# Kernel tuning notes

Hardware: AMD Instinct MI355X
Metric: run time of the kernel (lower is better)

## Reference

```python
import jax, jax.numpy as jnp
import numpy as np

EMBED_DIM = 1024
NUM_HEADS = 16
HEAD_DIM = EMBED_DIM // NUM_HEADS
STD = 0.02


def setup_inputs() -> dict:
    key = jax.random.key(0)
    k1, k2, k3 = jax.random.split(key, 3)
    B, S = 2, 2048
    inputs = jax.random.normal(k1, (B, S, EMBED_DIM), dtype=jnp.float32)
    # qkv projection: Linear(E, 3E); torch Linear weight is [out, in]
    w_qkv = jax.random.normal(k2, (3 * EMBED_DIM, EMBED_DIM), dtype=jnp.float32) * STD
    b_qkv = jnp.zeros((3 * EMBED_DIM,), dtype=jnp.float32)
    w_out = jax.random.normal(k3, (EMBED_DIM, EMBED_DIM), dtype=jnp.float32) * STD
    b_out = jnp.zeros((EMBED_DIM,), dtype=jnp.float32)
    return {"inputs": inputs, "w_qkv": w_qkv, "b_qkv": b_qkv, "w_out": w_out, "b_out": b_out}


def reference(inputs, w_qkv, b_qkv, w_out, b_out):
    B, S, E = inputs.shape
    qkv = inputs @ w_qkv.T + b_qkv                      # [B,S,3E]
    q, k, v = jnp.split(qkv, 3, axis=2)                 # each [B,S,E]

    def split_heads(t):
        return t.reshape(B, S, NUM_HEADS, HEAD_DIM).transpose(0, 2, 1, 3)  # [B,H,S,D]

    q, k, v = split_heads(q), split_heads(k), split_heads(v)
    scores = jnp.einsum('bhqd,bhkd->bhqk', q, k) * (1.0 / np.sqrt(HEAD_DIM))
    causal = jnp.tril(jnp.ones((S, S), dtype=bool))     # [S,S]
    scores = jnp.where(causal[None, None, :, :], scores, -jnp.inf)
    probs = jax.nn.softmax(scores, axis=-1)             # dropout is identity in eval mode
    ctx = jnp.einsum('bhqk,bhkd->bhqd', probs, v)       # [B,H,S,D]
    ctx = ctx.transpose(0, 2, 1, 3).reshape(B, S, E)
    return ctx @ w_out.T + b_out
```

## Files before the change

kernel.cpp:

```cpp
#include <hip/hip_runtime.h>
#include <hip/hip_bf16.h>

#define BATCH 2
#define SEQ   2048
#define EMB   1024
#define NHEAD 16
#define HDIM  64
#define MTOT  (BATCH*SEQ)
#define KTOT  EMB

#define NX  (MTOT*EMB)
#define NW1 (3*EMB*EMB)
#define NW2 (EMB*EMB)
#define NCVT (NX+NW1+NW2)

typedef short bf8 __attribute__((ext_vector_type(8)));
typedef short s4v __attribute__((ext_vector_type(4)));
typedef float f4  __attribute__((ext_vector_type(4)));
typedef unsigned int uint;

__device__ __forceinline__ short f2b(float f) {
    __hip_bfloat16 h = __float2bfloat16(f);
    return __builtin_bit_cast(short, h);
}
__device__ __forceinline__ void gl_lds16(const short* g, short* l) {
    __builtin_amdgcn_global_load_lds(
        (const __attribute__((address_space(1))) uint*)g,
        (__attribute__((address_space(3))) uint*)l, 16, 0, 0);
}
#define SWZ_SRC(lane)      ((((lane) ^ ((lane)>>2) ^ ((lane)>>4)) & 3) * 8)
#define SWZ_RD(quad, l16)  ((((quad) ^ (l16) ^ ((l16)>>2)) & 3) * 8)

__global__ __launch_bounds__(256) void cvt_all(
    const float* __restrict__ X, const float* __restrict__ W1,
    const float* __restrict__ W2,
    short* __restrict__ xb, short* __restrict__ w1b, short* __restrict__ w2b)
{
    int i4 = (blockIdx.x * 256 + threadIdx.x) * 4;
    const float* src; short* dst; int off;
    if (i4 < NX)            { src = X;  dst = xb;  off = i4; }
    else if (i4 < NX + NW1) { src = W1; dst = w1b; off = i4 - NX; }
    else                    { src = W2; dst = w2b; off = i4 - NX - NW1; }
    float4 v = *(const float4*)&src[off];
    s4v o; o[0]=f2b(v.x); o[1]=f2b(v.y); o[2]=f2b(v.z); o[3]=f2b(v.w);
    *(s4v*)&dst[off] = o;
}

__global__ __launch_bounds__(256) void gemm_qkv(
    const short* __restrict__ Xb, const short* __restrict__ Wb,
    const float* __restrict__ bias,
    short* __restrict__ qb, short* __restrict__ kb, short* __restrict__ vtb)
{
    __shared__ __align__(16) short As[2*128*32];
    __shared__ __align__(16) short Bs[2*128*32];
    const int tid  = threadIdx.x;
    const int lane = tid & 63;
    const int w    = tid >> 6;
    const int l16  = lane & 15, quad = lane >> 4;
    const int wm   = (w >> 1) * 64, wn = (w & 1) * 64;
    const int srow = (lane >> 2);
    const int scol = SWZ_SRC(lane);

    const int id  = blockIdx.x;
    const int xcd = id & 7, k = id >> 3;
    const int rg  = k / 12, p = k - rg*12;
    const int R   = rg*8 + xcd;
    const int bm  = (R & 7)*4 + (p & 3);
    const int bn  = (R >> 3)*3 + (p >> 2);

    f4 acc[4][4] = {};
    for (int k0 = 0; k0 < KTOT; k0 += 64) {
        #pragma unroll
        for (int t = 0; t < 4; t++) {
            const int rr = w*32 + (t & 1)*16;
            const int kc = t >> 1;
            int ra = bm*128 + rr + srow;
            gl_lds16(&Xb[(size_t)ra*KTOT + k0 + kc*32 + scol], &As[kc*4096 + rr*32]);
            int rb = bn*128 + rr + srow;
            gl_lds16(&Wb[(size_t)rb*KTOT + k0 + kc*32 + scol], &Bs[kc*4096 + rr*32]);
        }
        __syncthreads();
        #pragma unroll
        for (int kc = 0; kc < 2; kc++) {
            bf8 af[4], bf[4];
            #pragma unroll
            for (int t = 0; t < 4; t++) {
                af[t] = *(const bf8*)&As[kc*4096 + (wm + t*16 + l16)*32 + SWZ_RD(quad, l16)];
                bf[t] = *(const bf8*)&Bs[kc*4096 + (wn + t*16 + l16)*32 + SWZ_RD(quad, l16)];
            }
            #pragma unroll
            for (int mt = 0; mt < 4; mt++)
                #pragma unroll
                for (int nt = 0; nt < 4; nt++)
                    acc[mt][nt] = __builtin_amdgcn_mfma_f32_16x16x32_bf16(af[mt], bf[nt], acc[mt][nt], 0, 0, 0);
        }
        __syncthreads();
    }
    #pragma unroll
    for (int mt = 0; mt < 4; mt++)
    #pragma unroll
    for (int nt = 0; nt < 4; nt++) {
        int colg = bn*128 + wn + nt*16 + l16;
        float bv = bias[colg];
        #pragma unroll
        for (int r = 0; r < 4; r++) {
            int rowg = bm*128 + wm + mt*16 + quad*4 + r;
            short h = f2b(acc[mt][nt][r] + bv);
            int bb = rowg >> 11, s = rowg & 2047;
            if (colg < 1024) {
                int hh = colg >> 6, d = colg & 63;
                qb[(((bb*NHEAD + hh)*SEQ + s) << 6) + d] = h;
            } else if (colg < 2048) {
                int c2 = colg - 1024, hh = c2 >> 6, d = c2 & 63;
                kb[(((bb*NHEAD + hh)*SEQ + s) << 6) + d] = h;
            } else {
                int c3 = colg - 2048, hh = c3 >> 6, d = c3 & 63;
                int ssw = (s & ~63) | (((s & 15) << 2) | ((s >> 4) & 3));
                vtb[((bb*NHEAD + hh)*HDIM + d)*SEQ + ssw] = h;
            }
        }
    }
}

__global__ __launch_bounds__(256, 4) void attn(
    const short* __restrict__ qb, const short* __restrict__ kb,
    const short* __restrict__ vtb, short* __restrict__ ctx)
{
    __shared__ __align__(16) short Ks[2*4096];
    __shared__ __align__(16) short Vs[2*4096];
    __shared__ __align__(16) short pl[4][16*64];
    const int tid = threadIdx.x;
    const int w = tid >> 6, lane = tid & 63;
    const int l16 = lane & 15, quad = lane >> 4;
    const int f  = blockIdx.x;
    const int xcd = f & 7, j = f >> 3;
    const int bh  = xcd*4 + (j & 3);
    const int slot = j >> 2;
    const int j5 = slot & 7;
    const int hq = slot >> 3;
    const int tq = (hq == 0) ? j5 : (hq == 1) ? (15 - j5)
                 : (hq == 2) ? (16 + j5) : (31 - j5);
    const int q0w = tq*64 + w*16;
    const int base = bh * (SEQ*HDIM);
    short* myp = pl[w];
    const float SC = 0.125f * 1.44269504f;

    const int lq  = lane >> 2;
    const int lsw = SWZ_SRC(lane);

    const bool isk = (w < 2);
    short* tb = isk ? Ks : Vs;
    const int sstep = isk ? 64*HDIM : 64;
    const short* sp0; const short* sp1; const short* sp2; const short* sp3;
    int dof[4];
    {
        const int wb2 = (w & 1) * 4;
        #pragma unroll
        for (int tt = 0; tt < 4; tt++) {
            int t = wb2 + tt, cc = t & 1, g = (t >> 1) & 3;
            dof[tt] = (cc*64 + g*16)*32;
            const short* s = isk ? &kb[base + (g*16 + lq)*HDIM + cc*32 + lsw]
                                 : &vtb[base + (g*16 + lq)*SEQ + cc*32 + lsw];
            if (tt == 0) sp0 = s; else if (tt == 1) sp1 = s;
            else if (tt == 2) sp2 = s; else sp3 = s;
        }
    }

    bf8 qa[2];
    #pragma unroll
    for (int kc = 0; kc < 2; kc++)
        qa[kc] = *(const bf8*)&qb[base + (q0w + l16)*HDIM + kc*32 + quad*8];

    f4 o[4] = {};
    float lacc[4] = {};
    const int rdK = l16*32 + SWZ_RD(quad, l16);

    gl_lds16(sp0, tb + dof[0]); gl_lds16(sp1, tb + dof[1]);
    gl_lds16(sp2, tb + dof[2]); gl_lds16(sp3, tb + dof[3]);
    sp0 += sstep; sp1 += sstep; sp2 += sstep; sp3 += sstep;
    __syncthreads();

    int buf = 0;
    for (int st = 0; st <= tq; st++) {
        if (st < tq) {
            short* d = tb + (buf ^ 1)*4096;
            gl_lds16(sp0, d + dof[0]); gl_lds16(sp1, d + dof[1]);
            gl_lds16(sp2, d + dof[2]); gl_lds16(sp3, d + dof[3]);
            sp0 += sstep; sp1 += sstep; sp2 += sstep; sp3 += sstep;
        }
        const int kbase = buf*4096 + rdK;
        f4 s[4] = {};
        #pragma unroll
        for (int kf = 0; kf < 4; kf++)
            #pragma unroll
            for (int c = 0; c < 2; c++) {
                bf8 kfr = *(const bf8*)&Ks[kbase + (c*64 + kf*16)*32];
                s[kf] = __builtin_amdgcn_mfma_f32_16x16x32_bf16(qa[c], kfr, s[kf], 0, 0, 0);
            }
        if (st == tq) {
            const int j0 = st*64;
            #pragma unroll
            for (int r = 0; r < 4; r++) {
                const int row = quad*4 + r;
                const int qi  = q0w + row;
                float e[4];
                #pragma unroll
                for (int kf = 0; kf < 4; kf++) {
                    e[kf] = __builtin_amdgcn_exp2f(s[kf][r] * SC);
                    if (j0 + kf*16 + l16 > qi) e[kf] = 0.0f;
                    lacc[r] += e[kf];
                }
                uint u01 = __builtin_amdgcn_perm(__builtin_bit_cast(uint, e[1]),
                                                 __builtin_bit_cast(uint, e[0]), 0x07060302u);
                uint u23 = __builtin_amdgcn_perm(__builtin_bit_cast(uint, e[3]),
                                                 __builtin_bit_cast(uint, e[2]), 0x07060302u);
                uint2 pk = {u01, u23};
                int c8 = ((l16 >> 1) ^ (row & 7));
                *(uint2*)&myp[row*64 + c8*8 + (l16 & 1)*4] = pk;
            }
        } else {
            #pragma unroll
            for (int r = 0; r < 4; r++) {
                const int row = quad*4 + r;
                float e[4];
                #pragma unroll
                for (int kf = 0; kf < 4; kf++) {
                    e[kf] = __builtin_amdgcn_exp2f(s[kf][r] * SC);
                    lacc[r] += e[kf];
                }
                uint u01 = __builtin_amdgcn_perm(__builtin_bit_cast(uint, e[1]),
                                                 __builtin_bit_cast(uint, e[0]), 0x07060302u);
                uint u23 = __builtin_amdgcn_perm(__builtin_bit_cast(uint, e[3]),
                                                 __builtin_bit_cast(uint, e[2]), 0x07060302u);
                uint2 pk = {u01, u23};
                int c8 = ((l16 >> 1) ^ (row & 7));
                *(uint2*)&myp[row*64 + c8*8 + (l16 & 1)*4] = pk;
            }
        }
        asm volatile("" ::: "memory");
        bf8 pa[2];
        #pragma unroll
        for (int kc = 0; kc < 2; kc++)
            pa[kc] = *(const bf8*)&myp[l16*64 + (((kc*4 + quad) ^ (l16 & 7)))*8];
        #pragma unroll
        for (int dt = 0; dt < 4; dt++)
            #pragma unroll
            for (int c = 0; c < 2; c++) {
                bf8 vf = *(const bf8*)&Vs[kbase + (c*64 + dt*16)*32];
                o[dt] = __builtin_amdgcn_mfma_f32_16x16x32_bf16(pa[c], vf, o[dt], 0, 0, 0);
            }
        __syncthreads();
        buf ^= 1;
    }
    #pragma unroll
    for (int r = 0; r < 4; r++) {
        float v = lacc[r];
        v += __shfl_xor(v, 1);
        v += __shfl_xor(v, 2);
        v += __shfl_xor(v, 4);
        v += __shfl_xor(v, 8);
        lacc[r] = v;
    }
    const int b = bh >> 4, h = bh & 15;
    #pragma unroll
    for (int r = 0; r < 4; r++) {
        float inv = 1.0f / lacc[r];
        int qi = q0w + quad*4 + r;
        int rowoff = (b*SEQ + qi)*EMB + h*HDIM;
        #pragma unroll
        for (int dt = 0; dt < 4; dt++)
            ctx[rowoff + dt*16 + l16] = f2b(o[dt][r] * inv);
    }
}

__global__ __launch_bounds__(256) void gemm_out(
    const short* __restrict__ A, const short* __restrict__ Wb,
    const float* __restrict__ bias, float* __restrict__ out)
{
    __shared__ __align__(16) short As[2*128*32];
    __shared__ __align__(16) short Bs[2*64*32];
    const int f = blockIdx.x;
    const int xcd = f & 7, j = f >> 3;
    const int bm  = (xcd & 3)*8 + (j & 7);
    const int bn  = (xcd >> 2)*8 + (j >> 3);
    const int tid  = threadIdx.x;
    const int lane = tid & 63;
    const int w    = tid >> 6;
    const int l16  = lane & 15, quad = lane >> 4;
    const int wm   = (w >> 1) * 64, wn = (w & 1) * 32;
    const int srow = (lane >> 2);
    const int scol = SWZ_SRC(lane);
    f4 acc[4][2] = {};
    for (int k0 = 0; k0 < KTOT; k0 += 64) {
        #pragma unroll
        for (int t = 0; t < 4; t++) {
            const int a  = w*4 + t;
            const int kc = a & 1, g = a >> 1;
            int ra = bm*128 + g*16 + srow;
            gl_lds16(&A[(size_t)ra*KTOT + k0 + kc*32 + scol], &As[kc*4096 + g*16*32]);
        }
        #pragma unroll
        for (int t = 0; t < 2; t++) {
            const int b  = w*2 + t;
            const int kc = b & 1, g = b >> 1;
            int rb = bn*64 + g*16 + srow;
            gl_lds16(&Wb[(size_t)rb*KTOT + k0 + kc*32 + scol], &Bs[kc*2048 + g*16*32]);
        }
        __syncthreads();
        #pragma unroll
        for (int kc = 0; kc < 2; kc++) {
            bf8 af[4], bf[2];
            #pragma unroll
            for (int t = 0; t < 4; t++)
                af[t] = *(const bf8*)&As[kc*4096 + (wm + t*16 + l16)*32 + SWZ_RD(quad, l16)];
            #pragma unroll
            for (int t = 0; t < 2; t++)
                bf[t] = *(const bf8*)&Bs[kc*2048 + (wn + t*16 + l16)*32 + SWZ_RD(quad, l16)];
            #pragma unroll
            for (int mt = 0; mt < 4; mt++)
                #pragma unroll
                for (int nt = 0; nt < 2; nt++)
                    acc[mt][nt] = __builtin_amdgcn_mfma_f32_16x16x32_bf16(af[mt], bf[nt], acc[mt][nt], 0, 0, 0);
        }
        __syncthreads();
    }
    #pragma unroll
    for (int mt = 0; mt < 4; mt++)
    #pragma unroll
    for (int nt = 0; nt < 2; nt++) {
        int colg = bn*64 + wn + nt*16 + l16;
        float bv = bias[colg];
        #pragma unroll
        for (int r = 0; r < 4; r++) {
            int rowg = bm*128 + wm + mt*16 + quad*4 + r;
            out[(size_t)rowg*EMB + colg] = acc[mt][nt][r] + bv;
        }
    }
}

extern "C" void kernel_launch(void* const* d_in, const int* in_sizes, int n_in,
                              void* d_out, int out_size, void* d_ws, size_t ws_size,
                              hipStream_t stream) {
    const float* X    = (const float*)d_in[0];
    const float* Wqkv = (const float*)d_in[1];
    const float* Bqkv = (const float*)d_in[2];
    const float* Wout = (const float*)d_in[3];
    const float* Bout = (const float*)d_in[4];
    float* out = (float*)d_out;

    short* xb    = (short*)d_ws;
    short* w1b   = xb  + NX;
    short* w2b   = w1b + NW1;
    short* qb    = w2b + NW2;
    short* kb    = qb  + NX;
    short* vtb   = kb  + NX;
    short* ctx   = vtb + NX;

    cvt_all<<<NCVT/1024, 256, 0, stream>>>(X, Wqkv, Wout, xb, w1b, w2b);
    gemm_qkv<<<dim3(768), 256, 0, stream>>>(xb, w1b, Bqkv, qb, kb, vtb);
    attn<<<dim3(1024), 256, 0, stream>>>(qb, kb, vtb, ctx);
    gemm_out<<<dim3(512), 256, 0, stream>>>(ctx, w2b, Bout, out);
}
```

Baseline: 175.2 us.

## Process two 64-row query groups per attention block to reuse K/V tiles

Each attention block now handles 128 query rows (two 64-row groups per block, one 16-row slice of each per wave) instead of 64, so every K/V tile loaded into LDS is used by both groups. The grid is halved to 512 blocks and the tile-to-block mapping is changed to pair short and long causal rows. This is meant to halve K/V global and LDS traffic per query. In exchange it uses more registers and LDS (occupancy hint lowered from 4 to 3), halves the number of blocks available to fill the GPU, and leaves the first group idle on the final key step.

```diff
diff --git a/kernel.cpp b/kernel.cpp
--- a/kernel.cpp
+++ b/kernel.cpp
@@ -122,13 +122,13 @@
     }
 }
 
-__global__ __launch_bounds__(256, 4) void attn(
+__global__ __launch_bounds__(256, 3) void attn(
     const short* __restrict__ qb, const short* __restrict__ kb,
     const short* __restrict__ vtb, short* __restrict__ ctx)
 {
     __shared__ __align__(16) short Ks[2*4096];
     __shared__ __align__(16) short Vs[2*4096];
-    __shared__ __align__(16) short pl[4][16*64];
+    __shared__ __align__(16) short pl[4][32*64];
     const int tid = threadIdx.x;
     const int w = tid >> 6, lane = tid & 63;
     const int l16 = lane & 15, quad = lane >> 4;
@@ -136,11 +136,10 @@
     const int xcd = f & 7, j = f >> 3;
     const int bh  = xcd*4 + (j & 3);
     const int slot = j >> 2;
-    const int j5 = slot & 7;
+    const int s3 = slot & 7;
     const int hq = slot >> 3;
-    const int tq = (hq == 0) ? j5 : (hq == 1) ? (15 - j5)
-                 : (hq == 2) ? (16 + j5) : (31 - j5);
-    const int q0w = tq*64 + w*16;
+    const int tq = hq ? (15 - s3) : s3;
+    const int q0w = tq*128 + w*16;
     const int base = bh * (SEQ*HDIM);
     short* myp = pl[w];
     const float SC = 0.125f * 1.44269504f;
@@ -166,14 +165,17 @@
         }
     }
 
-    bf8 qa[2];
-    #pragma unroll
-    for (int kc = 0; kc < 2; kc++)
-        qa[kc] = *(const bf8*)&qb[base + (q0w + l16)*HDIM + kc*32 + quad*8];
-
-    f4 o[4] = {};
-    float lacc[4] = {};
+    bf8 qa[2][2];
+    #pragma unroll
+    for (int rg = 0; rg < 2; rg++)
+        #pragma unroll
+        for (int kc = 0; kc < 2; kc++)
+            qa[rg][kc] = *(const bf8*)&qb[base + (q0w + rg*64 + l16)*HDIM + kc*32 + quad*8];
+
+    f4 oA[4] = {}, oB[4] = {};
+    float lacc[2][4] = {};
     const int rdK = l16*32 + SWZ_RD(quad, l16);
+    const int nst = 2*tq + 2;
 
     gl_lds16(sp0, tb + dof[0]); gl_lds16(sp1, tb + dof[1]);
     gl_lds16(sp2, tb + dof[2]); gl_lds16(sp3, tb + dof[3]);
@@ -181,96 +183,121 @@
     __syncthreads();
 
     int buf = 0;
-    for (int st = 0; st <= tq; st++) {
-        if (st < tq) {
+    for (int st = 0; st < nst; st++) {
+        if (st < nst - 1) {
             short* d = tb + (buf ^ 1)*4096;
             gl_lds16(sp0, d + dof[0]); gl_lds16(sp1, d + dof[1]);
             gl_lds16(sp2, d + dof[2]); gl_lds16(sp3, d + dof[3]);
             sp0 += sstep; sp1 += sstep; sp2 += sstep; sp3 += sstep;
         }
         const int kbase = buf*4096 + rdK;
-        f4 s[4] = {};
-        #pragma unroll
-        for (int kf = 0; kf < 4; kf++)
-            #pragma unroll
-            for (int c = 0; c < 2; c++) {
-                bf8 kfr = *(const bf8*)&Ks[kbase + (c*64 + kf*16)*32];
-                s[kf] = __builtin_amdgcn_mfma_f32_16x16x32_bf16(qa[c], kfr, s[kf], 0, 0, 0);
+        const bool rg0act = (st <= 2*tq);
+        #pragma unroll
+        for (int rg = 0; rg < 2; rg++) {
+            if (rg == 0 && !rg0act) continue;
+            f4 s[4] = {};
+            #pragma unroll
+            for (int kf = 0; kf < 4; kf++)
+                #pragma unroll
+                for (int c = 0; c < 2; c++) {
+                    bf8 kfr = *(const bf8*)&Ks[kbase + (c*64 + kf*16)*32];
+                    s[kf] = __builtin_amdgcn_mfma_f32_16x16x32_bf16(qa[rg][c], kfr, s[kf], 0, 0, 0);
+                }
+            const bool diag = (st == 2*tq + rg);
+            if (diag) {
+                const int j0 = st*64;
+                #pragma unroll
+                for (int r = 0; r < 4; r++) {
+                    const int row = quad*4 + r;
+                    const int qi  = q0w + rg*64 + row;
+                    float e[4];
+                    #pragma unroll
+                    for (int kf = 0; kf < 4; kf++) {
+                        e[kf] = __builtin_amdgcn_exp2f(s[kf][r] * SC);
+                        if (j0 + kf*16 + l16 > qi) e[kf] = 0.0f;
+                        lacc[rg][r] += e[kf];
+                    }
+                    uint u01 = __builtin_amdgcn_perm(__builtin_bit_cast(uint, e[1]),
+                                                     __builtin_bit_cast(uint, e[0]), 0x07060302u);
+                    uint u23 = __builtin_amdgcn_perm(__builtin_bit_cast(uint, e[3]),
+                                                     __builtin_bit_cast(uint, e[2]), 0x07060302u);
+                    uint2 pk = {u01, u23};
+                    int c8 = ((l16 >> 1) ^ (row & 7));
+                    *(uint2*)&myp[(rg*16 + row)*64 + c8*8 + (l16 & 1)*4] = pk;
+                }
+            } else {
+                #pragma unroll
+                for (int r = 0; r < 4; r++) {
+                    const int row = quad*4 + r;
+                    float e[4];
+                    #pragma unroll
+                    for (int kf = 0; kf < 4; kf++) {
+                        e[kf] = __builtin_amdgcn_exp2f(s[kf][r] * SC);
+                        lacc[rg][r] += e[kf];
+                    }
+                    uint u01 = __builtin_amdgcn_perm(__builtin_bit_cast(uint, e[1]),
+                                                     __builtin_bit_cast(uint, e[0]), 0x07060302u);
+                    uint u23 = __builtin_amdgcn_perm(__builtin_bit_cast(uint, e[3]),
+                                                     __builtin_bit_cast(uint, e[2]), 0x07060302u);
+                    uint2 pk = {u01, u23};
+                    int c8 = ((l16 >> 1) ^ (row & 7));
+                    *(uint2*)&myp[(rg*16 + row)*64 + c8*8 + (l16 & 1)*4] = pk;
+                }
             }
-        if (st == tq) {
-            const int j0 = st*64;
-            #pragma unroll
-            for (int r = 0; r < 4; r++) {
-                const int row = quad*4 + r;
-                const int qi  = q0w + row;
-                float e[4];
-                #pragma unroll
-                for (int kf = 0; kf < 4; kf++) {
-                    e[kf] = __builtin_amdgcn_exp2f(s[kf][r] * SC);
-                    if (j0 + kf*16 + l16 > qi) e[kf] = 0.0f;
-                    lacc[r] += e[kf];
-                }
-                uint u01 = __builtin_amdgcn_perm(__builtin_bit_cast(uint, e[1]),
-                                                 __builtin_bit_cast(uint, e[0]), 0x07060302u);
-                uint u23 = __builtin_amdgcn_perm(__builtin_bit_cast(uint, e[3]),
-                                                 __builtin_bit_cast(uint, e[2]), 0x07060302u);
-                uint2 pk = {u01, u23};
-                int c8 = ((l16 >> 1) ^ (row & 7));
-                *(uint2*)&myp[row*64 + c8*8 + (l16 & 1)*4] = pk;
-            }
-        } else {
-            #pragma unroll
-            for (int r = 0; r < 4; r++) {
-                const int row = quad*4 + r;
-                float e[4];
-                #pragma unroll
-                for (int kf = 0; kf < 4; kf++) {
-                    e[kf] = __builtin_amdgcn_exp2f(s[kf][r] * SC);
-                    lacc[r] += e[kf];
-                }
-                uint u01 = __builtin_amdgcn_perm(__builtin_bit_cast(uint, e[1]),
-                                                 __builtin_bit_cast(uint, e[0]), 0x07060302u);
-                uint u23 = __builtin_amdgcn_perm(__builtin_bit_cast(uint, e[3]),
-                                                 __builtin_bit_cast(uint, e[2]), 0x07060302u);
-                uint2 pk = {u01, u23};
-                int c8 = ((l16 >> 1) ^ (row & 7));
-                *(uint2*)&myp[row*64 + c8*8 + (l16 & 1)*4] = pk;
-            }
         }
         asm volatile("" ::: "memory");
-        bf8 pa[2];
-        #pragma unroll
-        for (int kc = 0; kc < 2; kc++)
-            pa[kc] = *(const bf8*)&myp[l16*64 + (((kc*4 + quad) ^ (l16 & 7)))*8];
-        #pragma unroll
-        for (int dt = 0; dt < 4; dt++)
-            #pragma unroll
-            for (int c = 0; c < 2; c++) {
-                bf8 vf = *(const bf8*)&Vs[kbase + (c*64 + dt*16)*32];
-                o[dt] = __builtin_amdgcn_mfma_f32_16x16x32_bf16(pa[c], vf, o[dt], 0, 0, 0);
-            }
+        if (rg0act) {
+            bf8 pa[2];
+            #pragma unroll
+            for (int kc = 0; kc < 2; kc++)
+                pa[kc] = *(const bf8*)&myp[l16*64 + (((kc*4 + quad) ^ (l16 & 7)))*8];
+            #pragma unroll
+            for (int dt = 0; dt < 4; dt++)
+                #pragma unroll
+                for (int c = 0; c < 2; c++) {
+                    bf8 vf = *(const bf8*)&Vs[kbase + (c*64 + dt*16)*32];
+                    oA[dt] = __builtin_amdgcn_mfma_f32_16x16x32_bf16(pa[c], vf, oA[dt], 0, 0, 0);
+                }
+        }
+        {
+            bf8 pa[2];
+            #pragma unroll
+            for (int kc = 0; kc < 2; kc++)
+                pa[kc] = *(const bf8*)&myp[(16 + l16)*64 + (((kc*4 + quad) ^ (l16 & 7)))*8];
+            #pragma unroll
+            for (int dt = 0; dt < 4; dt++)
+                #pragma unroll
+                for (int c = 0; c < 2; c++) {
+                    bf8 vf = *(const bf8*)&Vs[kbase + (c*64 + dt*16)*32];
+                    oB[dt] = __builtin_amdgcn_mfma_f32_16x16x32_bf16(pa[c], vf, oB[dt], 0, 0, 0);
+                }
+        }
         __syncthreads();
         buf ^= 1;
     }
     #pragma unroll
-    for (int r = 0; r < 4; r++) {
-        float v = lacc[r];
-        v += __shfl_xor(v, 1);
-        v += __shfl_xor(v, 2);
-        v += __shfl_xor(v, 4);
-        v += __shfl_xor(v, 8);
-        lacc[r] = v;
-    }
+    for (int rg = 0; rg < 2; rg++)
+        #pragma unroll
+        for (int r = 0; r < 4; r++) {
+            float v = lacc[rg][r];
+            v += __shfl_xor(v, 1);
+            v += __shfl_xor(v, 2);
+            v += __shfl_xor(v, 4);
+            v += __shfl_xor(v, 8);
+            lacc[rg][r] = v;
+        }
     const int b = bh >> 4, h = bh & 15;
     #pragma unroll
-    for (int r = 0; r < 4; r++) {
-        float inv = 1.0f / lacc[r];
-        int qi = q0w + quad*4 + r;
-        int rowoff = (b*SEQ + qi)*EMB + h*HDIM;
-        #pragma unroll
-        for (int dt = 0; dt < 4; dt++)
-            ctx[rowoff + dt*16 + l16] = f2b(o[dt][r] * inv);
-    }
+    for (int rg = 0; rg < 2; rg++)
+        #pragma unroll
+        for (int r = 0; r < 4; r++) {
+            float inv = 1.0f / lacc[rg][r];
+            int qi = q0w + rg*64 + quad*4 + r;
+            int rowoff = (b*SEQ + qi)*EMB + h*HDIM;
+            #pragma unroll
+            for (int dt = 0; dt < 4; dt++)
+                ctx[rowoff + dt*16 + l16] = f2b((rg ? oB[dt][r] : oA[dt][r]) * inv);
+        }
 }
 
 __global__ __launch_bounds__(256) void gemm_out(
@@ -358,6 +385,6 @@
 
     cvt_all<<<NCVT/1024, 256, 0, stream>>>(X, Wqkv, Wout, xb, w1b, w2b);
     gemm_qkv<<<dim3(768), 256, 0, stream>>>(xb, w1b, Bqkv, qb, kb, vtb);
-    attn<<<dim3(1024), 256, 0, stream>>>(qb, kb, vtb, ctx);
+    attn<<<dim3(512), 256, 0, stream>>>(qb, kb, vtb, ctx);
     gemm_out<<<dim3(512), 256, 0, stream>>>(ctx, w2b, Bout, out);
 }
```

Result: no change. 175.0 us, median of 2 (-0.1%).
